# Performance work log

Measured on AMD Instinct MI355X. Metric: run time of the kernel, lower is better.

## Reference

```python
import jax, jax.numpy as jnp
import numpy as np
from math import pi

FC_IN, FC_OUT = 64, 64
LABEL_NC = 35
B, C, H, W = 2, 64, 128, 128
EPS = 1e-5
SLOPE = 0.01  # torch leaky_relu default


def _pa(h, w):
    # absolute normalized coordinates, matches init_pos buffers
    xs = (jnp.arange(h, dtype=jnp.float32) / h) * 2.0 - 1.0
    ys = (jnp.arange(w, dtype=jnp.float32) / w) * 2.0 - 1.0
    px = jnp.broadcast_to(xs[:, None], (h, w))
    py = jnp.broadcast_to(ys[None, :], (h, w))
    return jnp.stack([px, py], 0)  # (2,h,w)


def _coords(h, w):
    # f0=3; while-loop runs once (f=3 -> f=1), so exactly 4 channels
    f = 3.0
    ang_x = 2.0 * pi * jnp.remainder(jnp.arange(w, dtype=jnp.float32), f) / f
    ang_y = 2.0 * pi * jnp.remainder(jnp.arange(h, dtype=jnp.float32), f) / f
    xcos = jnp.broadcast_to(jnp.cos(ang_x)[None, :], (h, w))
    xsin = jnp.broadcast_to(jnp.sin(ang_x)[None, :], (h, w))
    ycos = jnp.broadcast_to(jnp.cos(ang_y)[:, None], (h, w))
    ysin = jnp.broadcast_to(jnp.sin(ang_y)[:, None], (h, w))
    return jnp.stack([xcos, xsin, ycos, ysin], 0)  # (4,h,w)


def _nearest(t, h, w):
    # F.interpolate(mode='nearest') index map: floor(i*in/out)
    ih = jnp.arange(h) * t.shape[2] // h
    iw = jnp.arange(w) * t.shape[3] // w
    return t[:, :, ih][:, :, :, iw]


def setup_inputs() -> dict:
    key = jax.random.key(0)
    ks = jax.random.split(key, 7)
    return {
        "x": jax.random.normal(ks[0], (B, C, H, W), jnp.float32),
        "layout": jax.random.normal(ks[1], (B, LABEL_NC, H, W), jnp.float32),
        "pr": jax.random.normal(ks[2], (B, 2, H, W), jnp.float32),
        "conv_w": jax.random.normal(ks[3], (1, 10), jnp.float32) * 0.02,
        "conv_b": jnp.zeros((1,), jnp.float32),
        "W_table": jax.random.normal(ks[4], (LABEL_NC, FC_IN * FC_OUT), jnp.float32),
        "b_table": jax.random.normal(ks[5], (LABEL_NC, FC_OUT), jnp.float32) * 0.02,
        "pl": jax.random.normal(ks[6], (2, H, W), jnp.float32),
    }


def reference(x, layout, pr, conv_w, conv_b, W_table, b_table, pl):
    b, c, h, w = x.shape
    pa = jnp.broadcast_to(_pa(h, w)[None], (b, 2, h, w))
    plb = jnp.broadcast_to(pl[None], (b, 2, h, w))
    coords = jnp.broadcast_to(_coords(h, w)[None], (b, 4, h, w))
    prr = _nearest(pr, h, w)
    pos = jnp.concatenate([pa, plb, prr, coords], axis=1)  # (B,10,h,w)
    # 1x1 conv to a single channel, broadcast-added over C
    x = x + jnp.einsum('bchw,oc->bohw', pos, conv_w) + conv_b[None, :, None, None]
    # argmax-routed per-pixel affine params
    lay = _nearest(layout, h, w)
    arg = jnp.argmax(lay, axis=1)  # (B,h,w) int
    Wg = W_table[arg].reshape(b, h, w, FC_IN, FC_OUT)  # huge gathered tensor (as in original)
    bg = b_table[arg]  # (B,h,w,FC_OUT)
    xh = jnp.transpose(x, (0, 2, 3, 1))  # (B,h,w,C)
    y = jnp.einsum('bhwc,bhwco->bhwo', xh, Wg) + bg
    y = jnp.transpose(y, (0, 3, 1, 2))  # (B,FC_OUT,h,w)
    # instance norm (no affine, biased variance, eps=1e-5)
    mu = jnp.mean(y, axis=(2, 3), keepdims=True)
    var = jnp.var(y, axis=(2, 3), keepdims=True)
    y = (y - mu) * jax.lax.rsqrt(var + EPS)
    return jnp.where(y >= 0, y, SLOPE * y)
```

## Files before the change

kernel.cpp:

```cpp
#include <hip/hip_runtime.h>

#define HH 128
#define WW 128
#define CC 64
#define OO 64
#define NC 35
#define NPIX (HH*WW)

__global__ __launch_bounds__(256) void ky_kernel(
    const float* __restrict__ x, const float* __restrict__ layout,
    const float* __restrict__ pr, const float* __restrict__ cw,
    const float* __restrict__ cb, const float* __restrict__ Wt,
    const float* __restrict__ bt, const float* __restrict__ pl,
    float* __restrict__ out, float* __restrict__ sums)
{
    __shared__ float s_xh[64*65];
    __shared__ float s_y[64*65];
    __shared__ int   s_arg[64];
    __shared__ float s_red[4][64][2];

    const int t    = threadIdx.x;
    const int wv   = t >> 6;
    const int lane = t & 63;
    const int tile = blockIdx.x;
    const int b    = tile >> 8;
    const int rem  = tile & 255;
    const int h    = rem >> 1;
    const int w0   = (rem & 1) << 6;
    const int w    = w0 + lane;

    float pxv = (float)h * (2.0f/128.0f) - 1.0f;
    float pyv = (float)w * (2.0f/128.0f) - 1.0f;
    float pl0 = pl[h*WW + w];
    float pl1 = pl[NPIX + h*WW + w];
    float pr0 = pr[((b*2+0)*HH + h)*WW + w];
    float pr1 = pr[((b*2+1)*HH + h)*WW + w];
    int kx = w % 3, kyy = h % 3;
    const float C1 = -0.5f, S1 = 0.86602540378443864676f;
    float xcv = (kx==0)  ? 1.0f : C1;
    float xsv = (kx==0)  ? 0.0f : ((kx==1)  ? S1 : -S1);
    float ycv = (kyy==0) ? 1.0f : C1;
    float ysv = (kyy==0) ? 0.0f : ((kyy==1) ? S1 : -S1);
    float s = cb[0] + pxv*cw[0] + pyv*cw[1] + pl0*cw[2] + pl1*cw[3]
            + pr0*cw[4] + pr1*cw[5] + xcv*cw[6] + xsv*cw[7] + ycv*cw[8] + ysv*cw[9];

    #pragma unroll
    for (int k = 0; k < 16; ++k) {
        int c = wv*16 + k;
        s_xh[c*65 + lane] = x[((b*CC + c)*HH + h)*WW + w] + s;
    }

    if (wv == 0) {
        const float* lp = layout + ((size_t)b*NC*HH + h)*WW + w;
        float best = lp[0]; int bi = 0;
        #pragma unroll
        for (int c = 1; c < NC; ++c) {
            float v = lp[(size_t)c*NPIX];
            if (v > best) { best = v; bi = c; }
        }
        s_arg[lane] = bi;
    }
    __syncthreads();

    float sum_ = 0.f, ss_ = 0.f;
    for (int i = 0; i < 16; ++i) {
        int p = wv*16 + i;
        int l = s_arg[p];
        const float* Wl   = Wt + l*4096;
        const float* xcol = s_xh + p;
        float acc = bt[l*64 + lane];
        #pragma unroll 16
        for (int c = 0; c < 64; ++c)
            acc = fmaf(xcol[c*65], Wl[c*64 + lane], acc);
        s_y[p*65 + lane] = acc;
        sum_ += acc;
        ss_  += acc*acc;
    }
    s_red[wv][lane][0] = sum_;
    s_red[wv][lane][1] = ss_;
    __syncthreads();

    #pragma unroll
    for (int i = 0; i < 16; ++i) {
        int o = wv*16 + i;
        out[((b*OO + o)*HH + h)*WW + w0 + lane] = s_y[lane*65 + o];
    }

    if (wv == 0) {
        float S  = s_red[0][lane][0] + s_red[1][lane][0] + s_red[2][lane][0] + s_red[3][lane][0];
        float SS = s_red[0][lane][1] + s_red[1][lane][1] + s_red[2][lane][1] + s_red[3][lane][1];
        atomicAdd(&sums[(b*OO + lane)*2 + 0], S);
        atomicAdd(&sums[(b*OO + lane)*2 + 1], SS);
    }
}

__global__ __launch_bounds__(256) void norm_kernel(
    float* __restrict__ out, const float* __restrict__ sums)
{
    int idx = blockIdx.x * 256 + threadIdx.x;
    float4* o4 = reinterpret_cast<float4*>(out);
    float4 v = o4[idx];
    int bo = idx >> 12;
    float S  = sums[bo*2 + 0];
    float SS = sums[bo*2 + 1];
    const float invN = 1.0f/16384.0f;
    float mean = S * invN;
    float var  = SS * invN - mean*mean;
    float r    = rsqrtf(var + 1e-5f);
    float a;
    a = (v.x - mean) * r; v.x = (a >= 0.f) ? a : 0.01f*a;
    a = (v.y - mean) * r; v.y = (a >= 0.f) ? a : 0.01f*a;
    a = (v.z - mean) * r; v.z = (a >= 0.f) ? a : 0.01f*a;
    a = (v.w - mean) * r; v.w = (a >= 0.f) ? a : 0.01f*a;
    o4[idx] = v;
}

extern "C" void kernel_launch(void* const* d_in, const int* in_sizes, int n_in,
                              void* d_out, int out_size, void* d_ws, size_t ws_size,
                              hipStream_t stream) {
    const float* x      = (const float*)d_in[0];
    const float* layout = (const float*)d_in[1];
    const float* pr     = (const float*)d_in[2];
    const float* cw     = (const float*)d_in[3];
    const float* cb     = (const float*)d_in[4];
    const float* Wt     = (const float*)d_in[5];
    const float* bt     = (const float*)d_in[6];
    const float* pl     = (const float*)d_in[7];
    float* out  = (float*)d_out;
    float* sums = (float*)d_ws;

    hipMemsetAsync(sums, 0, 2*OO*2*sizeof(float), stream);
    ky_kernel<<<512, 256, 0, stream>>>(x, layout, pr, cw, cb, Wt, bt, pl, out, sums);
    norm_kernel<<<2048, 256, 0, stream>>>(out, sums);
}
```

Before: 111.1 us.

## Halve pixel tile, vectorize weight loads with split-K shuffle, replace atomics with partial sums

Tiles shrink to 32 pixels per block, giving 1024 blocks instead of 512. The GEMV now has each lane load float4 weight rows with a 4-way split over input channels, reduced by cross-lane shuffles. The position term is added on the fly from a per-pixel shared value. The global atomics and the memset are replaced by per-block partial sums, which a new stats kernel reduces before normalization. This aims to raise occupancy, cut load instruction count and remove atomic contention, at the cost of an extra kernel launch and some lanes idling after the shuffle reduction.

```diff
diff --git a/kernel.cpp b/kernel.cpp
--- a/kernel.cpp
+++ b/kernel.cpp
@@ -6,52 +6,54 @@
 #define OO 64
 #define NC 35
 #define NPIX (HH*WW)
+#define NBLK 1024
 
 __global__ __launch_bounds__(256) void ky_kernel(
     const float* __restrict__ x, const float* __restrict__ layout,
     const float* __restrict__ pr, const float* __restrict__ cw,
     const float* __restrict__ cb, const float* __restrict__ Wt,
     const float* __restrict__ bt, const float* __restrict__ pl,
-    float* __restrict__ out, float* __restrict__ sums)
+    float* __restrict__ out, float* __restrict__ psum, float* __restrict__ pss)
 {
-    __shared__ float s_xh[64*65];
-    __shared__ float s_y[64*65];
-    __shared__ int   s_arg[64];
+    __shared__ float s_xh[64*33];
+    __shared__ float s_y[64*33];
+    __shared__ float s_s[32];
+    __shared__ int   s_arg[32];
     __shared__ float s_red[4][64][2];
 
     const int t    = threadIdx.x;
     const int wv   = t >> 6;
     const int lane = t & 63;
+    const int i15  = lane & 15;
+    const int ihi  = lane >> 4;
     const int tile = blockIdx.x;
-    const int b    = tile >> 8;
-    const int rem  = tile & 255;
-    const int h    = rem >> 1;
-    const int w0   = (rem & 1) << 6;
-    const int w    = w0 + lane;
-
-    float pxv = (float)h * (2.0f/128.0f) - 1.0f;
-    float pyv = (float)w * (2.0f/128.0f) - 1.0f;
-    float pl0 = pl[h*WW + w];
-    float pl1 = pl[NPIX + h*WW + w];
-    float pr0 = pr[((b*2+0)*HH + h)*WW + w];
-    float pr1 = pr[((b*2+1)*HH + h)*WW + w];
-    int kx = w % 3, kyy = h % 3;
-    const float C1 = -0.5f, S1 = 0.86602540378443864676f;
-    float xcv = (kx==0)  ? 1.0f : C1;
-    float xsv = (kx==0)  ? 0.0f : ((kx==1)  ? S1 : -S1);
-    float ycv = (kyy==0) ? 1.0f : C1;
-    float ysv = (kyy==0) ? 0.0f : ((kyy==1) ? S1 : -S1);
-    float s = cb[0] + pxv*cw[0] + pyv*cw[1] + pl0*cw[2] + pl1*cw[3]
-            + pr0*cw[4] + pr1*cw[5] + xcv*cw[6] + xsv*cw[7] + ycv*cw[8] + ysv*cw[9];
-
-    #pragma unroll
-    for (int k = 0; k < 16; ++k) {
-        int c = wv*16 + k;
-        s_xh[c*65 + lane] = x[((b*CC + c)*HH + h)*WW + w] + s;
-    }
-
-    if (wv == 0) {
-        const float* lp = layout + ((size_t)b*NC*HH + h)*WW + w;
+    const int b    = tile >> 9;
+    const int rem  = tile & 511;
+    const int h    = rem >> 2;
+    const int w0   = (rem & 3) << 5;
+
+    if (wv == 0 && lane < 32) {
+        int w = w0 + lane;
+        float pxv = (float)h * (2.0f/128.0f) - 1.0f;
+        float pyv = (float)w * (2.0f/128.0f) - 1.0f;
+        float pl0 = pl[h*WW + w];
+        float pl1 = pl[NPIX + h*WW + w];
+        float pr0 = pr[((b*2+0)*HH + h)*WW + w];
+        float pr1 = pr[((b*2+1)*HH + h)*WW + w];
+        int kx = w % 3, kyy = h % 3;
+        const float C1 = -0.5f, S1 = 0.86602540378443864676f;
+        float xcv = (kx==0)  ? 1.0f : C1;
+        float xsv = (kx==0)  ? 0.0f : ((kx==1)  ? S1 : -S1);
+        float ycv = (kyy==0) ? 1.0f : C1;
+        float ysv = (kyy==0) ? 0.0f : ((kyy==1) ? S1 : -S1);
+        s_s[lane] = cb[0] + pxv*cw[0] + pyv*cw[1] + pl0*cw[2] + pl1*cw[3]
+                  + pr0*cw[4] + pr1*cw[5] + xcv*cw[6] + xsv*cw[7]
+                  + ycv*cw[8] + ysv*cw[9];
+    }
+
+    if (wv == 1 && lane < 32) {
+        int w = w0 + lane;
+        const float* lp = layout + ((size_t)(b*NC)*HH + h)*WW + w;
         float best = lp[0]; int bi = 0;
         #pragma unroll
         for (int c = 1; c < NC; ++c) {
@@ -60,53 +62,118 @@
         }
         s_arg[lane] = bi;
     }
+
+    {
+        int p = t & 31, c0 = t >> 5;
+        const float* xp = x + ((size_t)(b*CC)*HH + h)*WW + w0 + p;
+        #pragma unroll
+        for (int k = 0; k < 8; ++k) {
+            int c = c0 + 8*k;
+            s_xh[c*33 + p] = xp[(size_t)c*NPIX];
+        }
+    }
     __syncthreads();
 
-    float sum_ = 0.f, ss_ = 0.f;
-    for (int i = 0; i < 16; ++i) {
-        int p = wv*16 + i;
+    float4 sumv = {0,0,0,0}, ssv = {0,0,0,0};
+    for (int i = 0; i < 8; ++i) {
+        int p = wv*8 + i;
         int l = s_arg[p];
-        const float* Wl   = Wt + l*4096;
-        const float* xcol = s_xh + p;
-        float acc = bt[l*64 + lane];
-        #pragma unroll 16
-        for (int c = 0; c < 64; ++c)
-            acc = fmaf(xcol[c*65], Wl[c*64 + lane], acc);
-        s_y[p*65 + lane] = acc;
-        sum_ += acc;
-        ss_  += acc*acc;
-    }
-    s_red[wv][lane][0] = sum_;
-    s_red[wv][lane][1] = ss_;
+        float sp = s_s[p];
+        const float4* W4 = (const float4*)(Wt + l*4096) + lane;
+        float4 a = {0,0,0,0};
+        #pragma unroll
+        for (int tt = 0; tt < 16; ++tt) {
+            float4 q  = W4[tt*64];
+            float  xv = s_xh[(4*tt + ihi)*33 + p] + sp;
+            a.x = fmaf(xv, q.x, a.x);
+            a.y = fmaf(xv, q.y, a.y);
+            a.z = fmaf(xv, q.z, a.z);
+            a.w = fmaf(xv, q.w, a.w);
+        }
+        a.x += __shfl_xor(a.x, 16); a.y += __shfl_xor(a.y, 16);
+        a.z += __shfl_xor(a.z, 16); a.w += __shfl_xor(a.w, 16);
+        a.x += __shfl_xor(a.x, 32); a.y += __shfl_xor(a.y, 32);
+        a.z += __shfl_xor(a.z, 32); a.w += __shfl_xor(a.w, 32);
+        if (ihi == 0) {
+            float4 bq = ((const float4*)(bt + l*64))[i15];
+            float y0 = a.x + bq.x, y1 = a.y + bq.y;
+            float y2 = a.z + bq.z, y3 = a.w + bq.w;
+            int o = 4*i15;
+            s_y[(o+0)*33 + p] = y0;
+            s_y[(o+1)*33 + p] = y1;
+            s_y[(o+2)*33 + p] = y2;
+            s_y[(o+3)*33 + p] = y3;
+            sumv.x += y0; ssv.x += y0*y0;
+            sumv.y += y1; ssv.y += y1*y1;
+            sumv.z += y2; ssv.z += y2*y2;
+            sumv.w += y3; ssv.w += y3*y3;
+        }
+    }
+    if (ihi == 0) {
+        int o = 4*i15;
+        s_red[wv][o+0][0] = sumv.x; s_red[wv][o+0][1] = ssv.x;
+        s_red[wv][o+1][0] = sumv.y; s_red[wv][o+1][1] = ssv.y;
+        s_red[wv][o+2][0] = sumv.z; s_red[wv][o+2][1] = ssv.z;
+        s_red[wv][o+3][0] = sumv.w; s_red[wv][o+3][1] = ssv.w;
+    }
     __syncthreads();
 
-    #pragma unroll
-    for (int i = 0; i < 16; ++i) {
-        int o = wv*16 + i;
-        out[((b*OO + o)*HH + h)*WW + w0 + lane] = s_y[lane*65 + o];
+    {
+        int p = t & 31, o0 = t >> 5;
+        float* op = out + ((size_t)(b*OO)*HH + h)*WW + w0 + p;
+        #pragma unroll
+        for (int k = 0; k < 8; ++k) {
+            int o = o0 + 8*k;
+            op[(size_t)o*NPIX] = s_y[o*33 + p];
+        }
     }
 
     if (wv == 0) {
         float S  = s_red[0][lane][0] + s_red[1][lane][0] + s_red[2][lane][0] + s_red[3][lane][0];
         float SS = s_red[0][lane][1] + s_red[1][lane][1] + s_red[2][lane][1] + s_red[3][lane][1];
-        atomicAdd(&sums[(b*OO + lane)*2 + 0], S);
-        atomicAdd(&sums[(b*OO + lane)*2 + 1], SS);
+        psum[lane*NBLK + tile] = S;
+        pss [lane*NBLK + tile] = SS;
+    }
+}
+
+__global__ __launch_bounds__(256) void stats_kernel(
+    const float* __restrict__ psum, const float* __restrict__ pss,
+    float* __restrict__ stats)
+{
+    __shared__ float2 red[256];
+    int e = blockIdx.x;
+    int b = e >> 6, o = e & 63;
+    int t = threadIdx.x;
+    const float* ps = psum + o*NBLK + b*512;
+    const float* pq = pss  + o*NBLK + b*512;
+    float2 v;
+    v.x = ps[t] + ps[t+256];
+    v.y = pq[t] + pq[t+256];
+    red[t] = v;
+    __syncthreads();
+    #pragma unroll
+    for (int s = 128; s > 0; s >>= 1) {
+        if (t < s) { red[t].x += red[t+s].x; red[t].y += red[t+s].y; }
+        __syncthreads();
+    }
+    if (t == 0) {
+        const float invN = 1.0f/16384.0f;
+        float mean = red[0].x * invN;
+        float var  = red[0].y * invN - mean*mean;
+        stats[e*2+0] = mean;
+        stats[e*2+1] = rsqrtf(var + 1e-5f);
     }
 }
 
 __global__ __launch_bounds__(256) void norm_kernel(
-    float* __restrict__ out, const float* __restrict__ sums)
+    float* __restrict__ out, const float* __restrict__ stats)
 {
     int idx = blockIdx.x * 256 + threadIdx.x;
     float4* o4 = reinterpret_cast<float4*>(out);
     float4 v = o4[idx];
     int bo = idx >> 12;
-    float S  = sums[bo*2 + 0];
-    float SS = sums[bo*2 + 1];
-    const float invN = 1.0f/16384.0f;
-    float mean = S * invN;
-    float var  = SS * invN - mean*mean;
-    float r    = rsqrtf(var + 1e-5f);
+    float mean = stats[bo*2 + 0];
+    float r    = stats[bo*2 + 1];
     float a;
     a = (v.x - mean) * r; v.x = (a >= 0.f) ? a : 0.01f*a;
     a = (v.y - mean) * r; v.y = (a >= 0.f) ? a : 0.01f*a;
@@ -126,10 +193,12 @@
     const float* Wt     = (const float*)d_in[5];
     const float* bt     = (const float*)d_in[6];
     const float* pl     = (const float*)d_in[7];
-    float* out  = (float*)d_out;
-    float* sums = (float*)d_ws;
-
-    hipMemsetAsync(sums, 0, 2*OO*2*sizeof(float), stream);
-    ky_kernel<<<512, 256, 0, stream>>>(x, layout, pr, cw, cb, Wt, bt, pl, out, sums);
-    norm_kernel<<<2048, 256, 0, stream>>>(out, sums);
-}
+    float* out   = (float*)d_out;
+    float* psum  = (float*)d_ws;
+    float* pss   = psum + (size_t)OO*NBLK;
+    float* stats = pss  + (size_t)OO*NBLK;
+
+    ky_kernel<<<NBLK, 256, 0, stream>>>(x, layout, pr, cw, cb, Wt, bt, pl, out, psum, pss);
+    stats_kernel<<<128, 256, 0, stream>>>(psum, pss, stats);
+    norm_kernel<<<2048, 256, 0, stream>>>(out, stats);
+}
```

Result: faster. 102.8 us (-7.4%).

## Bucket pixels by argmax label and run per-label GEMM with register-held weights

Applied to the files above, without the earlier changes.

Splits the work into three kernels. A prep kernel adds the positional term and writes a pixel-major copy of x, computes the argmax label and appends each pixel to a per-(batch,label) list via atomics. A GEMM kernel then processes one label chunk at a time with that label's weight column held in registers, so the weight table is no longer re-read from cache for every pixel. A norm kernel transposes the results back while applying instance norm and leaky ReLU. In exchange it adds extra global round trips for the x and y intermediates and launches many blocks that exit early. It also silently drops pixels if one label exceeds the fixed per-label capacity of 4096.

```diff
diff --git a/kernel.cpp b/kernel.cpp
--- a/kernel.cpp
+++ b/kernel.cpp
@@ -2,117 +2,199 @@
 
 #define HH 128
 #define WW 128
-#define CC 64
-#define OO 64
+#define NPIX (HH*WW)
 #define NC 35
-#define NPIX (HH*WW)
-
-__global__ __launch_bounds__(256) void ky_kernel(
+#define CAP 4096
+#define NCHUNK 64
+
+__global__ __launch_bounds__(256) void prep_kernel(
     const float* __restrict__ x, const float* __restrict__ layout,
     const float* __restrict__ pr, const float* __restrict__ cw,
-    const float* __restrict__ cb, const float* __restrict__ Wt,
-    const float* __restrict__ bt, const float* __restrict__ pl,
-    float* __restrict__ out, float* __restrict__ sums)
+    const float* __restrict__ cb, const float* __restrict__ pl,
+    float* __restrict__ xt, int* __restrict__ cnt, int* __restrict__ list)
 {
-    __shared__ float s_xh[64*65];
-    __shared__ float s_y[64*65];
-    __shared__ int   s_arg[64];
-    __shared__ float s_red[4][64][2];
-
-    const int t    = threadIdx.x;
-    const int wv   = t >> 6;
-    const int lane = t & 63;
-    const int tile = blockIdx.x;
-    const int b    = tile >> 8;
-    const int rem  = tile & 255;
-    const int h    = rem >> 1;
-    const int w0   = (rem & 1) << 6;
-    const int w    = w0 + lane;
-
-    float pxv = (float)h * (2.0f/128.0f) - 1.0f;
-    float pyv = (float)w * (2.0f/128.0f) - 1.0f;
-    float pl0 = pl[h*WW + w];
-    float pl1 = pl[NPIX + h*WW + w];
-    float pr0 = pr[((b*2+0)*HH + h)*WW + w];
-    float pr1 = pr[((b*2+1)*HH + h)*WW + w];
-    int kx = w % 3, kyy = h % 3;
-    const float C1 = -0.5f, S1 = 0.86602540378443864676f;
-    float xcv = (kx==0)  ? 1.0f : C1;
-    float xsv = (kx==0)  ? 0.0f : ((kx==1)  ? S1 : -S1);
-    float ycv = (kyy==0) ? 1.0f : C1;
-    float ysv = (kyy==0) ? 0.0f : ((kyy==1) ? S1 : -S1);
-    float s = cb[0] + pxv*cw[0] + pyv*cw[1] + pl0*cw[2] + pl1*cw[3]
-            + pr0*cw[4] + pr1*cw[5] + xcv*cw[6] + xsv*cw[7] + ycv*cw[8] + ysv*cw[9];
-
-    #pragma unroll
-    for (int k = 0; k < 16; ++k) {
-        int c = wv*16 + k;
-        s_xh[c*65 + lane] = x[((b*CC + c)*HH + h)*WW + w] + s;
-    }
-
-    if (wv == 0) {
-        const float* lp = layout + ((size_t)b*NC*HH + h)*WW + w;
+    __shared__ float s_t[64*65];
+    __shared__ float s_s[64];
+
+    const int t  = threadIdx.x;
+    const int bk = blockIdx.x;
+    const int b  = bk >> 8;
+    const int p0 = (bk & 255) << 6;
+    const int h  = p0 >> 7;
+    const int w0 = p0 & 127;
+
+    const float4* x4 = (const float4*)x + (size_t)b*64*4096 + (p0 >> 2);
+    #pragma unroll
+    for (int k = 0; k < 4; ++k) {
+        int f = k*256 + t;
+        int c = f >> 4, i = f & 15;
+        float4 q = x4[c*4096 + i];
+        int base = c*65 + i*4;
+        s_t[base+0]=q.x; s_t[base+1]=q.y; s_t[base+2]=q.z; s_t[base+3]=q.w;
+    }
+
+    if (t < 64) {
+        int w = w0 + t;
+        float pxv = (float)h * (2.0f/128.0f) - 1.0f;
+        float pyv = (float)w * (2.0f/128.0f) - 1.0f;
+        float pl0 = pl[h*WW + w];
+        float pl1 = pl[NPIX + h*WW + w];
+        float pr0 = pr[((b*2+0)*HH + h)*WW + w];
+        float pr1 = pr[((b*2+1)*HH + h)*WW + w];
+        int kx = w % 3, kyy = h % 3;
+        const float C1 = -0.5f, S1 = 0.86602540378443864676f;
+        float xcv = (kx==0)  ? 1.0f : C1;
+        float xsv = (kx==0)  ? 0.0f : ((kx==1)  ? S1 : -S1);
+        float ycv = (kyy==0) ? 1.0f : C1;
+        float ysv = (kyy==0) ? 0.0f : ((kyy==1) ? S1 : -S1);
+        s_s[t] = cb[0] + pxv*cw[0] + pyv*cw[1] + pl0*cw[2] + pl1*cw[3]
+               + pr0*cw[4] + pr1*cw[5] + xcv*cw[6] + xsv*cw[7]
+               + ycv*cw[8] + ysv*cw[9];
+    } else if (t < 128) {
+        int lane = t - 64;
+        const float* lp = layout + (size_t)(b*NC)*NPIX + p0 + lane;
         float best = lp[0]; int bi = 0;
         #pragma unroll
         for (int c = 1; c < NC; ++c) {
             float v = lp[(size_t)c*NPIX];
             if (v > best) { best = v; bi = c; }
         }
-        s_arg[lane] = bi;
-    }
-    __syncthreads();
-
-    float sum_ = 0.f, ss_ = 0.f;
+        int idx = atomicAdd(&cnt[b*NC + bi], 1);
+        if (idx < CAP) list[(b*NC + bi)*CAP + idx] = p0 + lane;
+    }
+    __syncthreads();
+
+    float4* xt4 = (float4*)xt + ((size_t)b*NPIX + p0)*16;
+    #pragma unroll
+    for (int k = 0; k < 4; ++k) {
+        int g = k*256 + t;
+        int p = g >> 4, c4 = g & 15;
+        float sp = s_s[p];
+        float4 q;
+        q.x = s_t[(c4*4+0)*65 + p] + sp;
+        q.y = s_t[(c4*4+1)*65 + p] + sp;
+        q.z = s_t[(c4*4+2)*65 + p] + sp;
+        q.w = s_t[(c4*4+3)*65 + p] + sp;
+        xt4[p*16 + c4] = q;
+    }
+}
+
+__global__ __launch_bounds__(256) void gemm_kernel(
+    const float* __restrict__ Wt, const float* __restrict__ bt,
+    const float* __restrict__ xt, const int* __restrict__ cnt,
+    const int* __restrict__ list, float* __restrict__ yt,
+    float* __restrict__ sums)
+{
+    const int bk    = blockIdx.x;
+    const int chunk = bk & (NCHUNK-1);
+    const int bl    = bk >> 6;
+    const int n     = cnt[bl];
+    const int base  = chunk * 64;
+    if (base >= n) return;
+    const int m = min(64, n - base);
+    const int b = bl / NC, l = bl % NC;
+
+    __shared__ float s_x[64*64];
+    __shared__ int   s_pix[64];
+    __shared__ float s_red[4][64][2];
+
+    const int t = threadIdx.x;
+    const int wv = t >> 6, lane = t & 63;
+
+    if (t < 64) s_pix[t] = (t < m) ? list[bl*CAP + base + t] : 0;
+    __syncthreads();
+
+    {
+        int p = t >> 2, j = t & 3;
+        if (p < m) {
+            const float4* r = (const float4*)xt + ((size_t)b*NPIX + s_pix[p])*16;
+            #pragma unroll
+            for (int k = 0; k < 4; ++k)
+                *((float4*)(s_x + p*64 + j*16 + k*4)) = r[j*4 + k];
+        }
+    }
+
+    float Wcol[64];
+    const float* Wl = Wt + l*4096 + lane;
+    #pragma unroll
+    for (int c = 0; c < 64; ++c) Wcol[c] = Wl[c*64];
+    float bias = bt[l*64 + lane];
+    __syncthreads();
+
+    float ssum = 0.f, sss = 0.f;
+    #pragma unroll 1
     for (int i = 0; i < 16; ++i) {
         int p = wv*16 + i;
-        int l = s_arg[p];
-        const float* Wl   = Wt + l*4096;
-        const float* xcol = s_xh + p;
-        float acc = bt[l*64 + lane];
-        #pragma unroll 16
-        for (int c = 0; c < 64; ++c)
-            acc = fmaf(xcol[c*65], Wl[c*64 + lane], acc);
-        s_y[p*65 + lane] = acc;
-        sum_ += acc;
-        ss_  += acc*acc;
-    }
-    s_red[wv][lane][0] = sum_;
-    s_red[wv][lane][1] = ss_;
-    __syncthreads();
-
-    #pragma unroll
-    for (int i = 0; i < 16; ++i) {
-        int o = wv*16 + i;
-        out[((b*OO + o)*HH + h)*WW + w0 + lane] = s_y[lane*65 + o];
-    }
-
+        if (p < m) {
+            float acc = bias;
+            const float4* xr = (const float4*)(s_x + p*64);
+            #pragma unroll
+            for (int c4 = 0; c4 < 16; ++c4) {
+                float4 xq = xr[c4];
+                acc = fmaf(xq.x, Wcol[4*c4+0], acc);
+                acc = fmaf(xq.y, Wcol[4*c4+1], acc);
+                acc = fmaf(xq.z, Wcol[4*c4+2], acc);
+                acc = fmaf(xq.w, Wcol[4*c4+3], acc);
+            }
+            yt[((size_t)b*NPIX + s_pix[p])*64 + lane] = acc;
+            ssum += acc; sss += acc*acc;
+        }
+    }
+    s_red[wv][lane][0] = ssum;
+    s_red[wv][lane][1] = sss;
+    __syncthreads();
     if (wv == 0) {
-        float S  = s_red[0][lane][0] + s_red[1][lane][0] + s_red[2][lane][0] + s_red[3][lane][0];
-        float SS = s_red[0][lane][1] + s_red[1][lane][1] + s_red[2][lane][1] + s_red[3][lane][1];
-        atomicAdd(&sums[(b*OO + lane)*2 + 0], S);
-        atomicAdd(&sums[(b*OO + lane)*2 + 1], SS);
+        float S  = s_red[0][lane][0]+s_red[1][lane][0]+s_red[2][lane][0]+s_red[3][lane][0];
+        float SS = s_red[0][lane][1]+s_red[1][lane][1]+s_red[2][lane][1]+s_red[3][lane][1];
+        atomicAdd(&sums[(b*64+lane)*2+0], S);
+        atomicAdd(&sums[(b*64+lane)*2+1], SS);
     }
 }
 
 __global__ __launch_bounds__(256) void norm_kernel(
-    float* __restrict__ out, const float* __restrict__ sums)
+    const float* __restrict__ yt, const float* __restrict__ sums,
+    float* __restrict__ out)
 {
-    int idx = blockIdx.x * 256 + threadIdx.x;
-    float4* o4 = reinterpret_cast<float4*>(out);
-    float4 v = o4[idx];
-    int bo = idx >> 12;
-    float S  = sums[bo*2 + 0];
-    float SS = sums[bo*2 + 1];
-    const float invN = 1.0f/16384.0f;
-    float mean = S * invN;
-    float var  = SS * invN - mean*mean;
-    float r    = rsqrtf(var + 1e-5f);
-    float a;
-    a = (v.x - mean) * r; v.x = (a >= 0.f) ? a : 0.01f*a;
-    a = (v.y - mean) * r; v.y = (a >= 0.f) ? a : 0.01f*a;
-    a = (v.z - mean) * r; v.z = (a >= 0.f) ? a : 0.01f*a;
-    a = (v.w - mean) * r; v.w = (a >= 0.f) ? a : 0.01f*a;
-    o4[idx] = v;
+    __shared__ float s_t[64*65];
+    __shared__ float s_mean[64], s_rstd[64];
+
+    const int t  = threadIdx.x;
+    const int bk = blockIdx.x;
+    const int b  = bk >> 8;
+    const int p0 = (bk & 255) << 6;
+
+    if (t < 64) {
+        float S  = sums[(b*64+t)*2+0];
+        float SS = sums[(b*64+t)*2+1];
+        const float invN = 1.0f/16384.0f;
+        float mean = S * invN;
+        float var  = SS * invN - mean*mean;
+        s_mean[t] = mean;
+        s_rstd[t] = rsqrtf(var + 1e-5f);
+    }
+
+    const float4* y4 = (const float4*)yt + ((size_t)b*NPIX + p0)*16;
+    #pragma unroll
+    for (int k = 0; k < 4; ++k) {
+        int g = k*256 + t;
+        int p = g >> 4, o4 = g & 15;
+        float4 q = y4[p*16 + o4];
+        int base = (o4*4)*65 + p;
+        s_t[base]     = q.x;
+        s_t[base+65]  = q.y;
+        s_t[base+130] = q.z;
+        s_t[base+195] = q.w;
+    }
+    __syncthreads();
+
+    const int p = t & 63, og = (t >> 6) * 16;
+    float* op = out + ((size_t)b*64 + og)*NPIX + p0 + p;
+    #pragma unroll
+    for (int kk = 0; kk < 16; ++kk) {
+        int o = og + kk;
+        float v = (s_t[o*65 + p] - s_mean[o]) * s_rstd[o];
+        op[(size_t)kk*NPIX] = (v >= 0.f) ? v : 0.01f*v;
+    }
 }
 
 extern "C" void kernel_launch(void* const* d_in, const int* in_sizes, int n_in,
@@ -126,10 +208,17 @@
     const float* Wt     = (const float*)d_in[5];
     const float* bt     = (const float*)d_in[6];
     const float* pl     = (const float*)d_in[7];
-    float* out  = (float*)d_out;
-    float* sums = (float*)d_ws;
-
-    hipMemsetAsync(sums, 0, 2*OO*2*sizeof(float), stream);
-    ky_kernel<<<512, 256, 0, stream>>>(x, layout, pr, cw, cb, Wt, bt, pl, out, sums);
-    norm_kernel<<<2048, 256, 0, stream>>>(out, sums);
-}
+    float* out = (float*)d_out;
+
+    char* ws = (char*)d_ws;
+    float* sums = (float*)ws;
+    int*   cnt  = (int*)(ws + 1024);
+    int*   list = (int*)(ws + 2048);
+    float* xt   = (float*)(ws + 2048 + (size_t)2*NC*CAP*4);
+    float* yt   = xt + (size_t)2*NPIX*64;
+
+    hipMemsetAsync(d_ws, 0, 2048, stream);
+    prep_kernel<<<512, 256, 0, stream>>>(x, layout, pr, cw, cb, pl, xt, cnt, list);
+    gemm_kernel<<<2*NC*NCHUNK, 256, 0, stream>>>(Wt, bt, xt, cnt, list, yt, sums);
+    norm_kernel<<<512, 256, 0, stream>>>(yt, sums, out);
+}
```

Measured after the change: 175.3 us. 1.58x slower.
